# Performance work log

Hardware: AMD Instinct MI355X
Metric: run time of the kernel (lower is better)

The kernel has to match this reference:

```python
import jax, jax.numpy as jnp
import numpy as np

N = 131072        # batch of spacetime points
IN_FEAT = 5       # modified spherical features
WIDTH = 128       # SmoothMLP width (config default)
DEPTH = 4         # hidden layers (config default); 1 input layer + 3 stacked hidden
CLIP = 1.0
EPS = 1e-8


def _init_mlp(key, in_dim, width, n_stack):
    ks = jax.random.split(key, 2 * (n_stack + 2))
    s_in = 1.0 / np.sqrt(in_dim)
    s_h = 1.0 / np.sqrt(width)
    W0 = jax.random.normal(ks[0], (in_dim, width), jnp.float32) * s_in
    b0 = jnp.zeros((width,), jnp.float32)
    Wh = jax.random.normal(ks[1], (n_stack, width, width), jnp.float32) * s_h
    bh = jnp.zeros((n_stack, width), jnp.float32)
    Wo = jax.random.normal(ks[2], (width, 1), jnp.float32) * s_h
    bo = jnp.zeros((1,), jnp.float32)
    return W0, b0, Wh, bh, Wo, bo


def setup_inputs() -> dict:
    key = jax.random.key(0)
    k_x, k_dp, k_ic = jax.random.split(key, 3)
    tx_cart = jax.random.normal(k_x, (N, 4), jnp.float32)
    # make times positive so the integration interval [0, t] is well posed
    tx_cart = tx_cart.at[:, 0].set(jnp.abs(tx_cart[:, 0]) + 0.1)
    dp = _init_mlp(k_dp, IN_FEAT + 1, WIDTH, DEPTH - 1)  # delta_phi net: [t, sph...]
    ic = _init_mlp(k_ic, IN_FEAT, WIDTH, DEPTH - 1)       # initial correction net
    names_dp = ["dp_W0", "dp_b0", "dp_Wh", "dp_bh", "dp_Wo", "dp_bo"]
    names_ic = ["ic_W0", "ic_b0", "ic_Wh", "ic_bh", "ic_Wo", "ic_bo"]
    out = {"tx_cart": tx_cart}
    out.update(dict(zip(names_dp, dp)))
    out.update(dict(zip(names_ic, ic)))
    return out


def _mlp(x, W0, b0, Wh, bh, Wo, bo):
    # SmoothMLP: tanh activations, scalar output. x: (..., in_dim)
    h = jnp.tanh(x @ W0 + b0)
    for i in range(Wh.shape[0]):  # fixed small layer count
        h = jnp.tanh(h @ Wh[i] + bh[i])
    return h @ Wo + bo  # (..., 1)


def _cart_to_mod_sph(x_cart):
    # Modified spherical coords with smooth radial compactification (clip):
    # [r/(clip+r), cos(theta), sin(theta), cos(phi), sin(phi)] -> 5 features
    x, y, z = x_cart[:, 0], x_cart[:, 1], x_cart[:, 2]
    r = jnp.sqrt(x * x + y * y + z * z + EPS)
    rho = jnp.sqrt(x * x + y * y + EPS)
    u = r / (CLIP + r)
    cos_t = z / r
    sin_t = rho / r
    cos_p = x / rho
    sin_p = y / rho
    return jnp.stack([u, cos_t, sin_t, cos_p, sin_p], axis=1)  # (N, 5)


# 3-point Gauss-Legendre nodes/weights on [-1, 1]
_GL_NODES = jnp.array([-np.sqrt(3.0 / 5.0), 0.0, np.sqrt(3.0 / 5.0)], jnp.float32)
_GL_WEIGHTS = jnp.array([5.0 / 9.0, 8.0 / 9.0, 5.0 / 9.0], jnp.float32)


def reference(tx_cart, dp_W0, dp_b0, dp_Wh, dp_bh, dp_Wo, dp_bo,
              ic_W0, ic_b0, ic_Wh, ic_bh, ic_Wo, ic_bo):
    t0 = 0.0
    t = tx_cart[:, 0]                        # (N,) per-row end time
    x_sph = _cart_to_mod_sph(tx_cart[:, 1:4])  # (N, 5)

    # initial correction at t0
    phi0 = _mlp(x_sph, ic_W0, ic_b0, ic_Wh, ic_bh, ic_Wo, ic_bo)[:, 0]  # (N,)

    # GL3 quadrature of d(phi)/dt over [t0, t] per row, fully vectorized
    a = (t - t0) * 0.5                       # (N,) half-width
    b = (t + t0) * 0.5                       # (N,) midpoint
    ts = a[:, None] * _GL_NODES[None, :] + b[:, None]          # (N, 3)
    sph_b = jnp.broadcast_to(x_sph[:, None, :], (x_sph.shape[0], 3, IN_FEAT))
    z = jnp.concatenate([ts[:, :, None], sph_b], axis=2)       # (N, 3, 6)
    vals = _mlp(z, dp_W0, dp_b0, dp_Wh, dp_bh, dp_Wo, dp_bo)[..., 0]  # (N, 3)
    delta_phi = a * jnp.sum(_GL_WEIGHTS * vals, axis=1)        # (N,)

    potential = phi0 + delta_phi
    return potential
```

## Files before the change

### kernel.cpp

```cpp
#include <hip/hip_runtime.h>

#define NPTS 131072
#define PPB  128
#define NBLK (NPTS / PPB)

#define FRAG0_OFF    0
#define FRAG0_BYTES  4096
#define FRAGH_OFF    4096
#define HLAYER_BYTES 32768
#define FRAGH_BYTES  (3 * HLAYER_BYTES)
#define BIAS_OFF     (FRAGH_OFF + FRAGH_BYTES)
#define BIAS_BYTES   2048
#define WO_OFF       (BIAS_OFF + BIAS_BYTES)
#define WOBO_BYTES   528
#define MLP_BYTES    (WO_OFF + WOBO_BYTES)

typedef _Float16 f16;
typedef __attribute__((ext_vector_type(8)))  _Float16 f16x8;
typedef __attribute__((ext_vector_type(16))) float    f32x16;

#define C2LOG2E 2.8853900817779268f

__device__ __forceinline__ float tanh_f(float x){
  float e = __builtin_amdgcn_exp2f(x * C2LOG2E);
  return 1.0f - 2.0f * __builtin_amdgcn_rcpf(e + 1.0f);
}

__device__ __forceinline__ void gl_lds16(const void* g, void* l){
  __builtin_amdgcn_global_load_lds(
      (const __attribute__((address_space(1))) void*)g,
      (__attribute__((address_space(3))) void*)l, 16, 0, 0);
}

__global__ void pack_weights(
    const float* __restrict__ dpW0, const float* __restrict__ dpb0,
    const float* __restrict__ dpWh, const float* __restrict__ dpbh,
    const float* __restrict__ dpWo, const float* __restrict__ dpbo,
    const float* __restrict__ icW0, const float* __restrict__ icb0,
    const float* __restrict__ icWh, const float* __restrict__ icbh,
    const float* __restrict__ icWo, const float* __restrict__ icbo,
    unsigned char* __restrict__ ws)
{
  int tid = blockIdx.x * blockDim.x + threadIdx.x;
  int nth = gridDim.x * blockDim.x;
  for (int m = 0; m < 2; ++m){
    const float* W0 = m ? icW0 : dpW0;
    const float* Wh = m ? icWh : dpWh;
    const float* b0 = m ? icb0 : dpb0;
    const float* bh = m ? icbh : dpbh;
    const float* Wo = m ? icWo : dpWo;
    const float* bo = m ? icbo : dpbo;
    const int indim = m ? 5 : 6;
    unsigned char* base = ws + m * MLP_BYTES;

    f16* dstF0 = (f16*)(base + FRAG0_OFF);
    for (int idx = tid; idx < 2048; idx += nth){
      int e    = idx & 7;
      int lane = (idx >> 3) & 63;
      int jt   = idx >> 9;
      int j = 32*jt + (lane & 31);
      int k = 8*(lane >> 5) + e;
      float v = (k < indim) ? W0[k*128 + j] : 0.0f;
      dstF0[idx] = (f16)v;
    }
    f16* dstFH = (f16*)(base + FRAGH_OFF);
    for (int idx = tid; idx < 3*16384; idx += nth){
      int layer = idx / 16384;
      int q     = idx & 16383;
      int e    = q & 7;
      int lane = (q >> 3) & 63;
      int f    = q >> 9;
      int jt = f >> 3, s = f & 7;
      int j = 32*jt + (lane & 31);
      int k = 16*s + 8*(lane >> 5) + e;
      int row = (k & ~12) | ((k & 4) << 1) | ((k & 8) >> 1);
      float v = Wh[(layer*128 + row)*128 + j];
      dstFH[idx] = (f16)v;
    }
    float* dstB = (float*)(base + BIAS_OFF);
    for (int idx = tid; idx < 512; idx += nth)
      dstB[idx] = (idx < 128) ? b0[idx] : bh[idx - 128];
    float* dstW = (float*)(base + WO_OFF);
    for (int idx = tid; idx < 128; idx += nth) dstW[idx] = Wo[idx];
    if (tid == 0) dstW[128] = bo[0];
  }
}

__device__ __forceinline__ f32x16 load_bias16(const float* bp){
  float4 q0 = *(const float4*)(bp +  0);
  float4 q1 = *(const float4*)(bp +  8);
  float4 q2 = *(const float4*)(bp + 16);
  float4 q3 = *(const float4*)(bp + 24);
  f32x16 a;
  a[0]=q0.x;  a[1]=q0.y;  a[2]=q0.z;  a[3]=q0.w;
  a[4]=q1.x;  a[5]=q1.y;  a[6]=q1.z;  a[7]=q1.w;
  a[8]=q2.x;  a[9]=q2.y;  a[10]=q2.z; a[11]=q2.w;
  a[12]=q3.x; a[13]=q3.y; a[14]=q3.z; a[15]=q3.w;
  return a;
}

__launch_bounds__(256, 4)
__global__ void node_main(const float* __restrict__ tx,
                          const unsigned char* __restrict__ ws,
                          float* __restrict__ out)
{
  __shared__ __align__(16) unsigned char sFrag[HLAYER_BYTES];
  __shared__ __align__(16) unsigned char sF0[FRAG0_BYTES];
  __shared__ __align__(16) float sBias[512];
  __shared__ __align__(16) float sWo[132];

  const int tid  = threadIdx.x;
  const int wave = tid >> 6;
  const int lane = tid & 63;
  const int p    = lane & 31;
  const int hi   = lane >> 5;
  const int gp   = blockIdx.x * PPB + wave * 32 + p;

  float4 c = ((const float4*)tx)[gp];
  float x = c.y, y = c.z, z = c.w;
  float xy = x*x + y*y;
  float r    = sqrtf(xy + z*z + 1e-8f);
  float rho  = sqrtf(xy + 1e-8f);
  float rin  = __builtin_amdgcn_rcpf(r);
  float rhin = __builtin_amdgcn_rcpf(rho);
  float u    = r * __builtin_amdgcn_rcpf(1.0f + r);
  float cth  = z * rin;
  float sth  = rho * rin;
  float cph  = x * rhin;
  float sph  = y * rhin;
  float th   = 0.5f * c.x;

  f32x16 acc[4];
  float vsum = 0.0f;

  #pragma unroll 1
  for (int chain = 0; chain < 4; ++chain){
    const unsigned char* mb = ws + ((chain == 3) ? MLP_BYTES : 0);

    if (chain == 0 || chain == 3){
      __syncthreads();
      gl_lds16(mb + FRAG0_OFF + wave*1024 + lane*16, sF0 + wave*1024);
      const uint4* s = (const uint4*)(mb + BIAS_OFF);
      for (int i = tid; i < 128; i += 256) ((uint4*)sBias)[i] = s[i];
      for (int i = tid; i < 33;  i += 256) ((uint4*)sWo)[i]   = s[128 + i];
      __syncthreads();
    }

    const float gn = (chain == 0) ? -0.7745966692414834f :
                     (chain == 2) ?  0.7745966692414834f : 0.0f;

    f16x8 b0f;
    #pragma unroll
    for (int e = 0; e < 8; ++e) b0f[e] = (f16)0.0f;
    if (hi == 0){
      if (chain == 3){
        b0f[0]=(f16)u;   b0f[1]=(f16)cth; b0f[2]=(f16)sth;
        b0f[3]=(f16)cph; b0f[4]=(f16)sph;
      } else {
        float ts = th * (1.0f + gn);
        b0f[0]=(f16)ts;  b0f[1]=(f16)u;   b0f[2]=(f16)cth;
        b0f[3]=(f16)sth; b0f[4]=(f16)cph; b0f[5]=(f16)sph;
      }
    }

    {
      const f16x8* fr = (const f16x8*)sF0;
      #pragma unroll
      for (int jt = 0; jt < 4; ++jt)
        acc[jt] = __builtin_amdgcn_mfma_f32_32x32x16_f16(
                    fr[jt*64 + lane], b0f,
                    load_bias16(&sBias[32*jt + 4*hi]), 0,0,0);
    }

    #pragma unroll 1
    for (int L = 0; L < 3; ++L){
      __syncthreads();
      {
        const unsigned char* src = mb + FRAGH_OFF + L*HLAYER_BYTES + wave*8192;
        unsigned char* dst = sFrag + wave*8192;
        #pragma unroll
        for (int i = 0; i < 8; ++i)
          gl_lds16(src + i*1024 + lane*16, dst + i*1024);
      }
      union { f16x8 v; unsigned uu[4]; } bf[8];
      #pragma unroll
      for (int jt = 0; jt < 4; ++jt)
        #pragma unroll
        for (int cq = 0; cq < 2; ++cq)
          #pragma unroll
          for (int e = 0; e < 4; ++e){
            float t0 = tanh_f(acc[jt][8*cq + 2*e]);
            float t1 = tanh_f(acc[jt][8*cq + 2*e + 1]);
            auto pk = __builtin_amdgcn_cvt_pkrtz(t0, t1);
            bf[2*jt + cq].uu[e] = __builtin_bit_cast(unsigned, pk);
          }
      __syncthreads();
      const f16x8* fh = (const f16x8*)sFrag;
      #pragma unroll
      for (int jt = 0; jt < 4; ++jt){
        f32x16 t = load_bias16(&sBias[(L+1)*128 + 32*jt + 4*hi]);
        #pragma unroll
        for (int s = 0; s < 8; ++s)
          t = __builtin_amdgcn_mfma_f32_32x32x16_f16(
                fh[(jt*8 + s)*64 + lane], bf[s].v, t, 0,0,0);
        acc[jt] = t;
      }
    }

    float v = 0.0f;
    #pragma unroll
    for (int jt = 0; jt < 4; ++jt){
      const float* wp = &sWo[32*jt + 4*hi];
      float4 q0 = *(const float4*)(wp +  0);
      float4 q1 = *(const float4*)(wp +  8);
      float4 q2 = *(const float4*)(wp + 16);
      float4 q3 = *(const float4*)(wp + 24);
      f32x16 A = acc[jt];
      v += tanh_f(A[0])*q0.x  + tanh_f(A[1])*q0.y
         + tanh_f(A[2])*q0.z  + tanh_f(A[3])*q0.w
         + tanh_f(A[4])*q1.x  + tanh_f(A[5])*q1.y
         + tanh_f(A[6])*q1.z  + tanh_f(A[7])*q1.w
         + tanh_f(A[8])*q2.x  + tanh_f(A[9])*q2.y
         + tanh_f(A[10])*q2.z + tanh_f(A[11])*q2.w
         + tanh_f(A[12])*q3.x + tanh_f(A[13])*q3.y
         + tanh_f(A[14])*q3.z + tanh_f(A[15])*q3.w;
    }
    v += __shfl_xor(v, 32);
    v += sWo[128];
    const float coeff = (chain == 3) ? 1.0f
                      : th * ((chain == 1) ? 0.8888888888888889f
                                           : 0.5555555555555556f);
    vsum = __builtin_fmaf(coeff, v, vsum);
  }

  if (hi == 0) out[gp] = vsum;
}

extern "C" void kernel_launch(void* const* d_in, const int* in_sizes, int n_in,
                              void* d_out, int out_size, void* d_ws, size_t ws_size,
                              hipStream_t stream)
{
  const float* tx = (const float*)d_in[0];
  pack_weights<<<64, 256, 0, stream>>>(
      (const float*)d_in[1],  (const float*)d_in[2],  (const float*)d_in[3],
      (const float*)d_in[4],  (const float*)d_in[5],  (const float*)d_in[6],
      (const float*)d_in[7],  (const float*)d_in[8],  (const float*)d_in[9],
      (const float*)d_in[10], (const float*)d_in[11], (const float*)d_in[12],
      (unsigned char*)d_ws);
  node_main<<<NBLK, 256, 0, stream>>>(tx, (const unsigned char*)d_ws, (float*)d_out);
}
```

Measured before the change: 93.72 us.

## Split quadrature nodes across blocks with resident weights and atomic accumulation

Each block now handles one of the four MLP evaluations (three GL nodes plus the initial-correction net) for a slice of points. It loads that net's full weight set into LDS once and loops over four batches of 512 points. Per-layer global-to-LDS reloads and their barriers go away. Partial results are combined with float atomics into a zeroed output. The cost is a memset, atomic traffic, order-dependent float summation, and a grid of only 256 blocks of 1024 threads each with about 100KB of LDS, so occupancy is lower.

```diff
diff --git a/kernel.cpp b/kernel.cpp
--- a/kernel.cpp
+++ b/kernel.cpp
@@ -1,14 +1,13 @@
 #include <hip/hip_runtime.h>
 
 #define NPTS 131072
-#define PPB  128
-#define NBLK (NPTS / PPB)
 
 #define FRAG0_OFF    0
 #define FRAG0_BYTES  4096
 #define FRAGH_OFF    4096
 #define HLAYER_BYTES 32768
 #define FRAGH_BYTES  (3 * HLAYER_BYTES)
+#define WCHUNKS      100
 #define BIAS_OFF     (FRAGH_OFF + FRAGH_BYTES)
 #define BIAS_BYTES   2048
 #define WO_OFF       (BIAS_OFF + BIAS_BYTES)
@@ -99,61 +98,59 @@
   return a;
 }
 
-__launch_bounds__(256, 4)
-__global__ void node_main(const float* __restrict__ tx,
-                          const unsigned char* __restrict__ ws,
-                          float* __restrict__ out)
+__global__ __launch_bounds__(1024) void node_main(
+    const float* __restrict__ tx,
+    const unsigned char* __restrict__ ws,
+    float* __restrict__ out)
 {
-  __shared__ __align__(16) unsigned char sFrag[HLAYER_BYTES];
-  __shared__ __align__(16) unsigned char sF0[FRAG0_BYTES];
+  __shared__ __align__(16) unsigned char sW[FRAG0_BYTES + FRAGH_BYTES];
   __shared__ __align__(16) float sBias[512];
-  __shared__ __align__(16) float sWo[132];
+  __shared__ __align__(16) float sWo[136];
 
   const int tid  = threadIdx.x;
   const int wave = tid >> 6;
   const int lane = tid & 63;
-  const int p    = lane & 31;
+  const int p32  = lane & 31;
   const int hi   = lane >> 5;
-  const int gp   = blockIdx.x * PPB + wave * 32 + p;
-
-  float4 c = ((const float4*)tx)[gp];
-  float x = c.y, y = c.z, z = c.w;
-  float xy = x*x + y*y;
-  float r    = sqrtf(xy + z*z + 1e-8f);
-  float rho  = sqrtf(xy + 1e-8f);
-  float rin  = __builtin_amdgcn_rcpf(r);
-  float rhin = __builtin_amdgcn_rcpf(rho);
-  float u    = r * __builtin_amdgcn_rcpf(1.0f + r);
-  float cth  = z * rin;
-  float sth  = rho * rin;
-  float cph  = x * rhin;
-  float sph  = y * rhin;
-  float th   = 0.5f * c.x;
-
-  f32x16 acc[4];
-  float vsum = 0.0f;
+  const int node = blockIdx.x >> 6;
+  const unsigned char* mb = ws + (node == 3 ? MLP_BYTES : 0);
+
+  for (int c = wave; c < WCHUNKS; c += 16)
+    gl_lds16(mb + c*1024 + lane*16, sW + c*1024);
+  for (int i = tid; i < 128; i += 1024)
+    ((uint4*)sBias)[i] = ((const uint4*)(mb + BIAS_OFF))[i];
+  for (int i = tid; i < 33; i += 1024)
+    ((uint4*)sWo)[i] = ((const uint4*)(mb + WO_OFF))[i];
+  __syncthreads();
+
+  const float gn = (node == 0) ? -0.7745966692414834f :
+                   (node == 2) ?  0.7745966692414834f : 0.0f;
+  const float wq = (node == 1) ? 0.8888888888888889f : 0.5555555555555556f;
 
   #pragma unroll 1
-  for (int chain = 0; chain < 4; ++chain){
-    const unsigned char* mb = ws + ((chain == 3) ? MLP_BYTES : 0);
-
-    if (chain == 0 || chain == 3){
-      __syncthreads();
-      gl_lds16(mb + FRAG0_OFF + wave*1024 + lane*16, sF0 + wave*1024);
-      const uint4* s = (const uint4*)(mb + BIAS_OFF);
-      for (int i = tid; i < 128; i += 256) ((uint4*)sBias)[i] = s[i];
-      for (int i = tid; i < 33;  i += 256) ((uint4*)sWo)[i]   = s[128 + i];
-      __syncthreads();
-    }
-
-    const float gn = (chain == 0) ? -0.7745966692414834f :
-                     (chain == 2) ?  0.7745966692414834f : 0.0f;
+  for (int u2 = 0; u2 < 4; ++u2){
+    const int batch = (blockIdx.x & 63) * 4 + u2;
+    const int p = batch * 512 + wave * 32 + p32;
+
+    float4 c = ((const float4*)tx)[p];
+    float x = c.y, y = c.z, z = c.w;
+    float xy = x*x + y*y;
+    float r    = sqrtf(xy + z*z + 1e-8f);
+    float rho  = sqrtf(xy + 1e-8f);
+    float rin  = __builtin_amdgcn_rcpf(r);
+    float rhin = __builtin_amdgcn_rcpf(rho);
+    float u    = r * __builtin_amdgcn_rcpf(1.0f + r);
+    float cth  = z * rin;
+    float sth  = rho * rin;
+    float cph  = x * rhin;
+    float sph  = y * rhin;
+    float th   = 0.5f * c.x;
 
     f16x8 b0f;
     #pragma unroll
     for (int e = 0; e < 8; ++e) b0f[e] = (f16)0.0f;
     if (hi == 0){
-      if (chain == 3){
+      if (node == 3){
         b0f[0]=(f16)u;   b0f[1]=(f16)cth; b0f[2]=(f16)sth;
         b0f[3]=(f16)cph; b0f[4]=(f16)sph;
       } else {
@@ -163,8 +160,9 @@
       }
     }
 
+    f32x16 acc[4];
     {
-      const f16x8* fr = (const f16x8*)sF0;
+      const f16x8* fr = (const f16x8*)sW;
       #pragma unroll
       for (int jt = 0; jt < 4; ++jt)
         acc[jt] = __builtin_amdgcn_mfma_f32_32x32x16_f16(
@@ -174,14 +172,6 @@
 
     #pragma unroll 1
     for (int L = 0; L < 3; ++L){
-      __syncthreads();
-      {
-        const unsigned char* src = mb + FRAGH_OFF + L*HLAYER_BYTES + wave*8192;
-        unsigned char* dst = sFrag + wave*8192;
-        #pragma unroll
-        for (int i = 0; i < 8; ++i)
-          gl_lds16(src + i*1024 + lane*16, dst + i*1024);
-      }
       union { f16x8 v; unsigned uu[4]; } bf[8];
       #pragma unroll
       for (int jt = 0; jt < 4; ++jt)
@@ -194,8 +184,7 @@
             auto pk = __builtin_amdgcn_cvt_pkrtz(t0, t1);
             bf[2*jt + cq].uu[e] = __builtin_bit_cast(unsigned, pk);
           }
-      __syncthreads();
-      const f16x8* fh = (const f16x8*)sFrag;
+      const f16x8* fh = (const f16x8*)(sW + FRAGH_OFF + L*HLAYER_BYTES);
       #pragma unroll
       for (int jt = 0; jt < 4; ++jt){
         f32x16 t = load_bias16(&sBias[(L+1)*128 + 32*jt + 4*hi]);
@@ -227,13 +216,9 @@
     }
     v += __shfl_xor(v, 32);
     v += sWo[128];
-    const float coeff = (chain == 3) ? 1.0f
-                      : th * ((chain == 1) ? 0.8888888888888889f
-                                           : 0.5555555555555556f);
-    vsum = __builtin_fmaf(coeff, v, vsum);
+    const float contrib = (node == 3) ? v : th * wq * v;
+    if (hi == 0) unsafeAtomicAdd(&out[p], contrib);
   }
-
-  if (hi == 0) out[gp] = vsum;
 }
 
 extern "C" void kernel_launch(void* const* d_in, const int* in_sizes, int n_in,
@@ -241,11 +226,12 @@
                               hipStream_t stream)
 {
   const float* tx = (const float*)d_in[0];
+  hipMemsetAsync(d_out, 0, (size_t)out_size * sizeof(float), stream);
   pack_weights<<<64, 256, 0, stream>>>(
       (const float*)d_in[1],  (const float*)d_in[2],  (const float*)d_in[3],
       (const float*)d_in[4],  (const float*)d_in[5],  (const float*)d_in[6],
       (const float*)d_in[7],  (const float*)d_in[8],  (const float*)d_in[9],
       (const float*)d_in[10], (const float*)d_in[11], (const float*)d_in[12],
       (unsigned char*)d_ws);
-  node_main<<<NBLK, 256, 0, stream>>>(tx, (const unsigned char*)d_ws, (float*)d_out);
-}
+  node_main<<<256, 1024, 0, stream>>>(tx, (const unsigned char*)d_ws, (float*)d_out);
+}
```

After: 135.0 us. 44.0% more time.
